# Performance work log

Hardware: AMD Instinct MI355X
Metric: run time of the kernel (lower is better)

## Reference

```python
import jax, jax.numpy as jnp
import numpy as np
import math

BATCH = 8192
INPUT_DIM = 4096
N_FEATURES = 2048
HAD = 4096  # 2**ceil(log2(max(input_dim, n_features)))
SCALE = math.sqrt(2.0 / N_FEATURES)
INV_SQRT_HAD = 1.0 / math.sqrt(HAD)


def fwht(x):
    """Fast Walsh-Hadamard transform, exact replica of the torch butterfly.
    x: [B, HAD] -> [B, HAD], scaled by 1/sqrt(HAD)."""
    B = x.shape[0]
    h = 1
    while h < HAD:  # log2(HAD) iterations, fixed at trace time
        x = x.reshape(B, -1, h, 2)
        x = jnp.concatenate([x[..., 0] + x[..., 1], x[..., 0] - x[..., 1]], axis=-1)
        x = x.reshape(B, -1)
        h *= 2
    return x * INV_SQRT_HAD


def setup_inputs() -> dict:
    key = jax.random.key(0)
    kx, k1, k2, k3, kp, kb = jax.random.split(key, 6)
    x = jax.random.normal(kx, (BATCH, INPUT_DIM), dtype=jnp.float32)
    D1 = jnp.sign(jax.random.normal(k1, (HAD,), dtype=jnp.float32))
    D2 = jnp.sign(jax.random.normal(k2, (HAD,), dtype=jnp.float32))
    D3 = jnp.sign(jax.random.normal(k3, (HAD,), dtype=jnp.float32))
    perm = jax.random.permutation(kp, HAD)
    bias = jax.random.uniform(kb, (N_FEATURES,), dtype=jnp.float32) * (2.0 * math.pi)
    return {"x": x, "D1": D1, "D2": D2, "D3": D3, "bias": bias, "perm": perm}


def reference(x, D1, D2, D3, bias, perm):
    # pad to hadamard_dim if needed (no-op here since INPUT_DIM == HAD)
    if x.shape[1] < HAD:
        x = jnp.pad(x, ((0, 0), (0, HAD - x.shape[1])))
    x = x * D1
    x = fwht(x)
    x = x * D2
    x = fwht(x)
    x = x * D3
    x = x[:, perm]          # random permutation of columns
    x = x[:, :N_FEATURES]   # keep first n_features columns
    return SCALE * jnp.cos(x + bias)
```

## Files before the change

### kernel.cpp

```cpp
#include <hip/hip_runtime.h>

#define HADN 4096
#define NFEAT 2048

__device__ __host__ __forceinline__ int pi_map(int q) {
  return  (((q >> 3) & 1))
        | (((q >> 11) & 1) << 1)
        | (((q >> 7) & 1) << 2)
        | (((q >> 1) & 1) << 3)
        | (((q >> 5) & 1) << 4)
        | (((q >> 9) & 1) << 5)
        | (((q >> 0) & 1) << 6)
        | (((q >> 2) & 1) << 7)
        | (((q >> 4) & 1) << 8)
        | (((q >> 6) & 1) << 9)
        | (((q >> 8) & 1) << 10)
        | (((q >> 10) & 1) << 11);
}

__device__ __host__ __forceinline__ int pi_inv_map(int p) {
  return  (((p >> 6) & 1))
        | (((p >> 3) & 1) << 1)
        | (((p >> 7) & 1) << 2)
        | (((p >> 0) & 1) << 3)
        | (((p >> 8) & 1) << 4)
        | (((p >> 4) & 1) << 5)
        | (((p >> 9) & 1) << 6)
        | (((p >> 2) & 1) << 7)
        | (((p >> 10) & 1) << 8)
        | (((p >> 5) & 1) << 9)
        | (((p >> 11) & 1) << 10)
        | (((p >> 1) & 1) << 11);
}

__device__ __forceinline__ int swz(int p) {
  return p ^ ((((p >> 6) ^ (p >> 9)) & 7) << 2);
}

template <int BIT>
__device__ __forceinline__ void bfly(float* r) {
#pragma unroll
  for (int e = 0; e < 16; ++e) {
    if ((e & BIT) == 0) {
      const int f = e | BIT;
      const float a = r[e], b = r[f];
      r[e] = a + b;
      r[f] = a - b;
    }
  }
}

__device__ __forceinline__ void shfl_bfly(float* r, int mask, bool upper) {
#pragma unroll
  for (int e = 0; e < 16; ++e) {
    const float v = __shfl_xor(r[e], mask, 64);
    r[e] = upper ? (v - r[e]) : (r[e] + v);
  }
}

__global__ __launch_bounds__(256) void srf_setup(
    const float* __restrict__ D2, const float* __restrict__ D3,
    const int* __restrict__ perm,
    float* __restrict__ D2p, float* __restrict__ d3g, int* __restrict__ gidx) {
  const int i = blockIdx.x * 256 + threadIdx.x;
  if (i < HADN) {
    D2p[i] = 0.25f * D2[pi_inv_map(i)];
  }
  if (i < NFEAT) {
    const int j = perm[i];
    gidx[i] = swz(pi_map(pi_map(j)));
    d3g[i] = 0.25f * D3[j];
  }
}

__global__ __launch_bounds__(256) void srf_main(
    const float* __restrict__ x, const float* __restrict__ D1,
    const float* __restrict__ D2p, const float* __restrict__ d3g,
    const int* __restrict__ gidx, const float* __restrict__ bias,
    float* __restrict__ out) {
  __shared__ float lds[HADN];
  const int tid = threadIdx.x;
  const long row = blockIdx.x;

  const float4* x4 = (const float4*)(x + row * HADN);
#pragma unroll
  for (int k = 0; k < 4; ++k) {
    const int c4 = k * 256 + tid;
    float4 v = x4[c4];
    const int p = c4 * 4;
    const float4 d = *(const float4*)(D1 + p);
    v.x *= d.x; v.y *= d.y; v.z *= d.z; v.w *= d.w;
    *(float4*)(&lds[swz(p)]) = v;
  }
  __syncthreads();

  {
    const int l = tid & 63;
    const int w = tid >> 6;
    const int base = ((l & 1) << 2) | (((l >> 1) & 1) << 5) | (((l >> 2) & 1) << 6)
                   | (((l >> 3) & 1) << 7) | (((l >> 4) & 1) << 8) | (((l >> 5) & 1) << 9)
                   | (w << 10);
    float r[16];
#pragma unroll
    for (int g = 0; g < 4; ++g) {
      const int p = base | ((g & 1) << 3) | (((g >> 1) & 1) << 4);
      const float4 v = *(const float4*)(&lds[swz(p)]);
      r[g * 4 + 0] = v.x; r[g * 4 + 1] = v.y; r[g * 4 + 2] = v.z; r[g * 4 + 3] = v.w;
    }
    bfly<2>(r); bfly<4>(r); bfly<8>(r);
    shfl_bfly(r, 2, (l & 2) != 0);
#pragma unroll
    for (int g = 0; g < 4; ++g) {
      const int p = base | ((g & 1) << 3) | (((g >> 1) & 1) << 4);
      const float4 d = *(const float4*)(D2p + p);
      r[g * 4 + 0] *= d.x; r[g * 4 + 1] *= d.y; r[g * 4 + 2] *= d.z; r[g * 4 + 3] *= d.w;
    }
    bfly<1>(r); bfly<4>(r); bfly<8>(r);
    shfl_bfly(r, 16, (l & 16) != 0);
#pragma unroll
    for (int g = 0; g < 4; ++g) {
      const int p = base | ((g & 1) << 3) | (((g >> 1) & 1) << 4);
      const float4 v = make_float4(r[g * 4 + 0], r[g * 4 + 1], r[g * 4 + 2], r[g * 4 + 3]);
      *(float4*)(&lds[swz(p)]) = v;
    }
  }
  __syncthreads();

#pragma unroll
  for (int j = 0; j < 2; ++j) {
    const int idx = j * 256 + tid;
    const int o = idx * 4;
    const int4 gi = *(const int4*)(gidx + o);
    const float4 dg = *(const float4*)(d3g + o);
    const float4 bz = *(const float4*)(bias + o);
    float4 res;
    res.x = 0.03125f * __cosf(lds[gi.x] * dg.x + bz.x);
    res.y = 0.03125f * __cosf(lds[gi.y] * dg.y + bz.y);
    res.z = 0.03125f * __cosf(lds[gi.z] * dg.z + bz.z);
    res.w = 0.03125f * __cosf(lds[gi.w] * dg.w + bz.w);
    *(float4*)(out + row * NFEAT + o) = res;
  }
}

extern "C" void kernel_launch(void* const* d_in, const int* in_sizes, int n_in,
                              void* d_out, int out_size, void* d_ws, size_t ws_size,
                              hipStream_t stream) {
  const float* x    = (const float*)d_in[0];
  const float* D1   = (const float*)d_in[1];
  const float* D2   = (const float*)d_in[2];
  const float* D3   = (const float*)d_in[3];
  const float* bias = (const float*)d_in[4];
  const int*   perm = (const int*)d_in[5];
  float* out = (float*)d_out;

  float* D2p = (float*)d_ws;
  float* d3g = D2p + HADN;
  int*   gidx = (int*)(d3g + NFEAT);

  srf_setup<<<16, 256, 0, stream>>>(D2, D3, perm, D2p, d3g, gidx);
  srf_main<<<8192, 256, 0, stream>>>(x, D1, D2p, d3g, gidx, bias, out);
}
```

Before: 46.41 us.

## Use DPP butterflies, bit-packed D2 sign flips, and nontemporal output stores

Replaces the cross-lane shuffle butterflies with DPP quad-permute operations by remapping lane-to-element bits so that the exchanged partners sit within a quad. The D2 diagonal is packed into sign bitmasks applied by XOR, and the 0.25 scale is folded into d3g. Output stores become nontemporal. This cuts LDS-backed shuffle traffic and D2 vector loads. The bit remapping has to stay consistent with the swizzle and permutation maps.

```diff
diff --git a/kernel.cpp b/kernel.cpp
--- a/kernel.cpp
+++ b/kernel.cpp
@@ -2,6 +2,8 @@
 
 #define HADN 4096
 #define NFEAT 2048
+
+typedef float floatx4 __attribute__((ext_vector_type(4)));
 
 __device__ __host__ __forceinline__ int pi_map(int q) {
   return  (((q >> 3) & 1))
@@ -50,32 +52,41 @@
   }
 }
 
-__device__ __forceinline__ void shfl_bfly(float* r, int mask, bool upper) {
+template <int CTRL>
+__device__ __forceinline__ void dpp_bfly(float* r, bool upper) {
+  const unsigned sm = upper ? 0x80000000u : 0u;
 #pragma unroll
   for (int e = 0; e < 16; ++e) {
-    const float v = __shfl_xor(r[e], mask, 64);
-    r[e] = upper ? (v - r[e]) : (r[e] + v);
+    const int pv = __builtin_amdgcn_update_dpp(
+        0, __float_as_int(r[e]), CTRL, 0xF, 0xF, true);
+    r[e] = __int_as_float(pv) + __int_as_float(__float_as_int(r[e]) ^ sm);
   }
 }
 
 __global__ __launch_bounds__(256) void srf_setup(
     const float* __restrict__ D2, const float* __restrict__ D3,
     const int* __restrict__ perm,
-    float* __restrict__ D2p, float* __restrict__ d3g, int* __restrict__ gidx) {
+    unsigned* __restrict__ D2sgn, float* __restrict__ d3g,
+    int* __restrict__ gidx) {
   const int i = blockIdx.x * 256 + threadIdx.x;
-  if (i < HADN) {
-    D2p[i] = 0.25f * D2[pi_inv_map(i)];
+  if (i < HADN / 32) {
+    unsigned wrd = 0;
+    for (int j = 0; j < 32; ++j) {
+      const int p = i * 32 + j;
+      wrd |= (__float_as_uint(D2[pi_inv_map(p)]) >> 31) << j;
+    }
+    D2sgn[i] = wrd;
   }
   if (i < NFEAT) {
     const int j = perm[i];
     gidx[i] = swz(pi_map(pi_map(j)));
-    d3g[i] = 0.25f * D3[j];
+    d3g[i] = 0.0625f * D3[j];
   }
 }
 
 __global__ __launch_bounds__(256) void srf_main(
     const float* __restrict__ x, const float* __restrict__ D1,
-    const float* __restrict__ D2p, const float* __restrict__ d3g,
+    const unsigned* __restrict__ D2sgn, const float* __restrict__ d3g,
     const int* __restrict__ gidx, const float* __restrict__ bias,
     float* __restrict__ out) {
   __shared__ float lds[HADN];
@@ -97,9 +108,9 @@
   {
     const int l = tid & 63;
     const int w = tid >> 6;
-    const int base = ((l & 1) << 2) | (((l >> 1) & 1) << 5) | (((l >> 2) & 1) << 6)
-                   | (((l >> 3) & 1) << 7) | (((l >> 4) & 1) << 8) | (((l >> 5) & 1) << 9)
-                   | (w << 10);
+    const int base = (((l >> 2) & 1) << 2) | ((l & 1) << 5) | (((l >> 3) & 1) << 6)
+                   | (((l >> 4) & 1) << 7) | (((l >> 1) & 1) << 8)
+                   | (((l >> 5) & 1) << 9) | (w << 10);
     float r[16];
 #pragma unroll
     for (int g = 0; g < 4; ++g) {
@@ -108,15 +119,18 @@
       r[g * 4 + 0] = v.x; r[g * 4 + 1] = v.y; r[g * 4 + 2] = v.z; r[g * 4 + 3] = v.w;
     }
     bfly<2>(r); bfly<4>(r); bfly<8>(r);
-    shfl_bfly(r, 2, (l & 2) != 0);
+    dpp_bfly<0xB1>(r, (l & 1) != 0);
+    {
+      const unsigned sw2 = D2sgn[base >> 5] >> (base & 4);
 #pragma unroll
-    for (int g = 0; g < 4; ++g) {
-      const int p = base | ((g & 1) << 3) | (((g >> 1) & 1) << 4);
-      const float4 d = *(const float4*)(D2p + p);
-      r[g * 4 + 0] *= d.x; r[g * 4 + 1] *= d.y; r[g * 4 + 2] *= d.z; r[g * 4 + 3] *= d.w;
+      for (int e = 0; e < 16; ++e) {
+        const int pos = (e & 3) | ((e & 12) << 1);
+        const unsigned m = (sw2 >> pos) << 31;
+        r[e] = __int_as_float(__float_as_int(r[e]) ^ m);
+      }
     }
     bfly<1>(r); bfly<4>(r); bfly<8>(r);
-    shfl_bfly(r, 16, (l & 16) != 0);
+    dpp_bfly<0x4E>(r, (l & 2) != 0);
 #pragma unroll
     for (int g = 0; g < 4; ++g) {
       const int p = base | ((g & 1) << 3) | (((g >> 1) & 1) << 4);
@@ -133,12 +147,12 @@
     const int4 gi = *(const int4*)(gidx + o);
     const float4 dg = *(const float4*)(d3g + o);
     const float4 bz = *(const float4*)(bias + o);
-    float4 res;
+    floatx4 res;
     res.x = 0.03125f * __cosf(lds[gi.x] * dg.x + bz.x);
     res.y = 0.03125f * __cosf(lds[gi.y] * dg.y + bz.y);
     res.z = 0.03125f * __cosf(lds[gi.z] * dg.z + bz.z);
     res.w = 0.03125f * __cosf(lds[gi.w] * dg.w + bz.w);
-    *(float4*)(out + row * NFEAT + o) = res;
+    __builtin_nontemporal_store(res, (floatx4*)(out + row * NFEAT + o));
   }
 }
 
@@ -153,10 +167,10 @@
   const int*   perm = (const int*)d_in[5];
   float* out = (float*)d_out;
 
-  float* D2p = (float*)d_ws;
-  float* d3g = D2p + HADN;
-  int*   gidx = (int*)(d3g + NFEAT);
+  unsigned* D2sgn = (unsigned*)d_ws;
+  float*    d3g   = (float*)(D2sgn + 128);
+  int*      gidx  = (int*)(d3g + NFEAT);
 
-  srf_setup<<<16, 256, 0, stream>>>(D2, D3, perm, D2p, d3g, gidx);
-  srf_main<<<8192, 256, 0, stream>>>(x, D1, D2p, d3g, gidx, bias, out);
+  srf_setup<<<8, 256, 0, stream>>>(D2, D3, perm, D2sgn, d3g, gidx);
+  srf_main<<<8192, 256, 0, stream>>>(x, D1, D2sgn, d3g, gidx, bias, out);
 }
```

Result: faster. 42.54 us (-8.3%).
